# Kernel optimization log

Measured on AMD Instinct MI355X. Metric: run time of the kernel, lower is better.

## Reference

```python
import jax, jax.numpy as jnp
import numpy as np

EPS = 1e-3  # keras LayerNormalization default epsilon


def setup_inputs() -> dict:
    key = jax.random.key(0)
    ks = jax.random.split(key, 6)
    B, T, D, U = 128, 512, 512, 512
    scale = 1.0 / np.sqrt(U + D)
    return {
        "x": jax.random.normal(ks[0], (B, T, D), jnp.float32),
        "h0": jnp.zeros((B, U), jnp.float32),
        "c0": jnp.zeros((B, U), jnp.float32),
        "Wf": jax.random.normal(ks[1], (U, U + D), jnp.float32) * scale,
        "bf": jnp.zeros((U,), jnp.float32),
        "Wg": jax.random.normal(ks[2], (U, U + D), jnp.float32) * scale,
        "bg": jnp.zeros((U,), jnp.float32),
        "Wi": jax.random.normal(ks[3], (U, U + D), jnp.float32) * scale,
        "bi": jnp.zeros((U,), jnp.float32),
        "Wo": jax.random.normal(ks[4], (U, U + D), jnp.float32) * scale,
        "bo": jnp.zeros((U,), jnp.float32),
        "gamma": jnp.ones((U,), jnp.float32),
        "beta": jnp.zeros((U,), jnp.float32),
    }


def reference(x, h0, c0, Wf, bf, Wg, bg, Wi, bi, Wo, bo, gamma, beta):
    # Stack the 4 gate weights/biases: one GEMM per step instead of four.
    W = jnp.stack([Wf, Wg, Wi, Wo])          # [4, U, U+D]
    b = jnp.stack([bf, bg, bi, bo])          # [4, U]

    def ln(z):
        # shared LayerNormalization over the last (units) axis
        m = jnp.mean(z, axis=-1, keepdims=True)
        v = jnp.var(z, axis=-1, keepdims=True)
        return (z - m) * jax.lax.rsqrt(v + EPS) * gamma + beta

    def step(carry, xt):
        h, c = carry                          # [B, U] each
        cat = jnp.concatenate([h, xt], axis=-1)   # [B, U+D]
        z = jnp.einsum('bd,gud->bgu', cat, W) + b  # [B, 4, U]
        z = ln(z)                             # LN per gate over units
        f = jax.nn.sigmoid(z[:, 0])
        g = jnp.tanh(z[:, 1])
        i = jax.nn.sigmoid(z[:, 2])
        o = jax.nn.sigmoid(z[:, 3])
        c_new = c * f + g * i
        c_ln = ln(c_new)                      # layer_norm_c_state: carried c is normalized
        h_new = o * jnp.tanh(c_ln)
        return (h_new, c_ln), h_new

    xs = jnp.swapaxes(x, 0, 1)                # [T, B, D]
    (_, _), hs = jax.lax.scan(step, (h0, c0), xs)
    return jnp.swapaxes(hs, 0, 1)             # [B, T, U]
```

## Files before the change

kernel.cpp:

```cpp
#include <hip/hip_runtime.h>
#include <hip/hip_fp16.h>


typedef unsigned short ushort_t;
typedef unsigned long long u64;
typedef __attribute__((ext_vector_type(8))) short short8;
typedef __attribute__((ext_vector_type(4))) float f32x4;

#define Bsz 128
#define Tn  512
#define Un  512
#define NU  2048
#define NC  16
#define WPC 16
#define BPC 8

#define GIDX(u) ((u) + ((u) >> 5))

__device__ __forceinline__ ushort_t f2bf(float f){
  unsigned u = __float_as_uint(f);
  u = u + 0x7fffu + ((u >> 16) & 1u);
  return (ushort_t)(u >> 16);
}
__device__ __forceinline__ float bf2f(ushort_t h){
  return __uint_as_float(((unsigned)h) << 16);
}
__device__ __forceinline__ float sigf(float x){ return 1.0f/(1.0f + __expf(-x)); }
__device__ __forceinline__ float tanh_fast(float x){
  float ax = fabsf(x);
  float e  = __expf(-2.0f*ax);
  float r  = (1.0f - e)/(1.0f + e);
  return x >= 0.0f ? r : -r;
}

__device__ __forceinline__ void st_tag(u64* p, float v, unsigned tag){
  u64 w = ((u64)tag << 32) | (u64)__float_as_uint(v);
  __hip_atomic_store(p, w, __ATOMIC_RELAXED, __HIP_MEMORY_SCOPE_AGENT);
}
__device__ __forceinline__ void st_u64(u64* p, u64 w){
  __hip_atomic_store(p, w, __ATOMIC_RELAXED, __HIP_MEMORY_SCOPE_AGENT);
}
__device__ __forceinline__ void st_f32(float* p, float v){
  __hip_atomic_store(p, v, __ATOMIC_RELAXED, __HIP_MEMORY_SCOPE_AGENT);
}
__device__ __forceinline__ u64 ld_u64(const u64* p){
  return __hip_atomic_load(p, __ATOMIC_RELAXED, __HIP_MEMORY_SCOPE_AGENT);
}
__device__ __forceinline__ float lo_f(u64 w){ return __uint_as_float((unsigned)w); }
__device__ __forceinline__ float hi_f(u64 w){ return __uint_as_float((unsigned)(w >> 32)); }

__global__ void k_prep_w(const float* __restrict__ Wf, const float* __restrict__ Wg,
                         const float* __restrict__ Wi, const float* __restrict__ Wo,
                         ushort_t* __restrict__ wh_hi, ushort_t* __restrict__ wh_lo){
  int idx = blockIdx.x*blockDim.x + threadIdx.x;
  if (idx >= 1048576) return;
  const float* Wp[4] = {Wf, Wg, Wi, Wo};
  int j = idx & 7;
  int lane = (idx >> 3) & 63;
  int i = (idx >> 9) & 31;
  int wslot = idx >> 14;
  int kiter = i >> 1, nt = i & 1;
  int wid = wslot >> 2, wave = wslot & 3;
  int n = wid*128 + wave*32 + nt*16 + (lane & 15);
  int k = kiter*32 + (lane >> 4)*8 + j;
  int gate = n >> 9, u = n & 511;
  float w = Wp[gate][u*1024 + k];
  ushort_t hi = f2bf(w);
  wh_hi[idx] = hi;
  wh_lo[idx] = f2bf(w - bf2f(hi));
}

__global__ __launch_bounds__(256,2) void k_gemm_xz(const float* __restrict__ A,
    const float* __restrict__ Wf, const float* __restrict__ Wg,
    const float* __restrict__ Wi, const float* __restrict__ Wo,
    __half* __restrict__ C){
  __shared__ __align__(16) ushort_t Ah[128*32];
  __shared__ __align__(16) ushort_t Al[128*32];
  __shared__ __align__(16) ushort_t Bh[128*32];
  __shared__ __align__(16) ushort_t Bl[128*32];
  const int tid  = threadIdx.x;
  const int lane = tid & 63, wave = tid >> 6;
  const int quad = lane >> 4, l15 = lane & 15;
  const int wm = wave >> 1, wn = wave & 1;
  const int m0 = blockIdx.x * 128, n0 = blockIdx.y * 128;
  const float* Wp = (n0 < 512) ? Wf : (n0 < 1024) ? Wg : (n0 < 1536) ? Wi : Wo;
  const int u0 = n0 & 511;
  f32x4 acc[4][4];
  #pragma unroll
  for (int a=0;a<4;a++)
    #pragma unroll
    for (int b=0;b<4;b++) acc[a][b] = (f32x4){0.f,0.f,0.f,0.f};

  for (int kc = 0; kc < 512; kc += 32){
    __syncthreads();
    #pragma unroll
    for (int p=0; p<4; p++){
      int slot = p*256 + tid;
      int row = slot >> 3, seg = slot & 7;
      float4 va = *(const float4*)(A  + (size_t)(m0+row)*512  + kc + seg*4);
      float4 vb = *(const float4*)(Wp + (size_t)(u0+row)*1024 + 512 + kc + seg*4);
      ushort4 ah, al, bh, bl;
      ah.x=f2bf(va.x); al.x=f2bf(va.x-bf2f(ah.x));
      ah.y=f2bf(va.y); al.y=f2bf(va.y-bf2f(ah.y));
      ah.z=f2bf(va.z); al.z=f2bf(va.z-bf2f(ah.z));
      ah.w=f2bf(va.w); al.w=f2bf(va.w-bf2f(ah.w));
      bh.x=f2bf(vb.x); bl.x=f2bf(vb.x-bf2f(bh.x));
      bh.y=f2bf(vb.y); bl.y=f2bf(vb.y-bf2f(bh.y));
      bh.z=f2bf(vb.z); bl.z=f2bf(vb.z-bf2f(bh.z));
      bh.w=f2bf(vb.w); bl.w=f2bf(vb.w-bf2f(bh.w));
      *(ushort4*)(Ah + slot*4) = ah;
      *(ushort4*)(Al + slot*4) = al;
      *(ushort4*)(Bh + slot*4) = bh;
      *(ushort4*)(Bl + slot*4) = bl;
    }
    __syncthreads();
    short8 afh[4], afl[4], bfh[4], bfl[4];
    #pragma unroll
    for (int ti=0; ti<4; ti++){
      afh[ti] = *(const short8*)(Ah + (wm*64 + ti*16 + l15)*32 + quad*8);
      afl[ti] = *(const short8*)(Al + (wm*64 + ti*16 + l15)*32 + quad*8);
    }
    #pragma unroll
    for (int tj=0; tj<4; tj++){
      bfh[tj] = *(const short8*)(Bh + (wn*64 + tj*16 + l15)*32 + quad*8);
      bfl[tj] = *(const short8*)(Bl + (wn*64 + tj*16 + l15)*32 + quad*8);
    }
    #pragma unroll
    for (int ti=0; ti<4; ti++)
      #pragma unroll
      for (int tj=0; tj<4; tj++){
        acc[ti][tj] = __builtin_amdgcn_mfma_f32_16x16x32_bf16(afh[ti], bfh[tj], acc[ti][tj], 0,0,0);
        acc[ti][tj] = __builtin_amdgcn_mfma_f32_16x16x32_bf16(afl[ti], bfh[tj], acc[ti][tj], 0,0,0);
        acc[ti][tj] = __builtin_amdgcn_mfma_f32_16x16x32_bf16(afh[ti], bfl[tj], acc[ti][tj], 0,0,0);
      }
  }
  #pragma unroll
  for (int ti=0; ti<4; ti++)
    #pragma unroll
    for (int tj=0; tj<4; tj++)
      #pragma unroll
      for (int r=0; r<4; r++){
        int m = m0 + wm*64 + ti*16 + quad*4 + r;
        int n = n0 + wn*64 + tj*16 + l15;
        C[(size_t)m*NU + n] = __float2half(acc[ti][tj][r]);
      }
}

__global__ __launch_bounds__(256,1) void k_lstm(
    const ushort_t* __restrict__ wh_hi_g, const ushort_t* __restrict__ wh_lo_g,
    const __half* __restrict__ xz,
    const float* __restrict__ bfp, const float* __restrict__ bgp,
    const float* __restrict__ bip, const float* __restrict__ bop,
    const float* __restrict__ gamma, const float* __restrict__ beta,
    const float* __restrict__ h0, const float* __restrict__ c0,
    float* __restrict__ actf, u64* __restrict__ zbuf,
    u64* __restrict__ zflag, u64* __restrict__ aflag,
    float* __restrict__ out)
{
  const int bid = blockIdx.x;
  const int cid = bid & 15;
  const int wid = bid >> 4;
  const int tid = threadIdx.x;
  const int wave = tid >> 6, lane = tid & 63;
  const int quad = lane >> 4, l15 = lane & 15;
  const int gate = wid >> 2;

  __shared__ __align__(16) ushort_t h_hi[16][520];
  __shared__ __align__(16) ushort_t h_lo[16][520];
  __shared__ float gamma_lds[528], beta_lds[528];
  __shared__ float wavepart[4][8][2];

  for (int i = tid; i < 16*520; i += 256){
    int r = i / 520, u = i - r*520;
    float v = (r < BPC && u < 512) ? h0[(cid*BPC + r)*512 + u] : 0.0f;
    ushort_t hh = f2bf(v);
    h_hi[r][u] = hh;
    h_lo[r][u] = f2bf(v - bf2f(hh));
  }
  for (int i = tid; i < 512; i += 256){ gamma_lds[GIDX(i)] = gamma[i]; beta_lds[GIDX(i)] = beta[i]; }

  const int b_loc = tid >> 5;
  const int l2 = (tid & 31) << 1;
  float c[16];
  #pragma unroll
  for (int i=0;i<16;i++) c[i] = c0[(cid*BPC + b_loc)*512 + (i>>1)*64 + l2 + (i&1)];

  short8 wrh[32], wrl[32];
  {
    const ushort_t* wph = wh_hi_g + (size_t)(wid*4 + wave)*16384 + lane*8;
    const ushort_t* wpl = wh_lo_g + (size_t)(wid*4 + wave)*16384 + lane*8;
    #pragma unroll
    for (int i=0;i<32;i++){
      wrh[i] = *(const short8*)(wph + (size_t)i*512);
      wrl[i] = *(const short8*)(wpl + (size_t)i*512);
    }
  }

  float bias_r[2], gam_r[2], bet_r[2];
  int ng_[2];
  #pragma unroll
  for (int nt=0; nt<2; nt++){
    int ng = wid*128 + wave*32 + nt*16 + l15;
    ng_[nt] = ng;
    int u = ng & 511;
    const float* bp = (gate==0)? bfp : (gate==1)? bgp : (gate==2)? bip : bop;
    bias_r[nt] = bp[u];
    gam_r[nt] = gamma[u]; bet_r[nt] = beta[u];
  }
  const bool bvalid = (quad < 2);
  const int b_base = quad*4;

  const size_t fbase0 = (size_t)(0*NC + cid)*WPC;
  const size_t fbase1 = (size_t)(1*NC + cid)*WPC;

  __syncthreads();

  for (int t = 0; t < Tn; ++t){
    const unsigned tag = (unsigned)(t + 1);
    const int par = t & 1;
    const size_t fb = par ? fbase1 : fbase0;
    float xzv[2][4];
    #pragma unroll
    for (int nt=0; nt<2; nt++)
      #pragma unroll
      for (int r=0; r<4; r++){
        if (bvalid){
          int b = cid*BPC + b_base + r;
          xzv[nt][r] = __half2float(xz[((size_t)b*Tn + t)*NU + ng_[nt]]);
        } else xzv[nt][r] = 0.0f;
      }
    f32x4 acc0 = (f32x4){0.f,0.f,0.f,0.f}, acc1 = (f32x4){0.f,0.f,0.f,0.f};
    #pragma unroll
    for (int ki=0; ki<16; ki++){
      short8 afh = *(const short8*)(&h_hi[l15][ki*32 + quad*8]);
      short8 afl = *(const short8*)(&h_lo[l15][ki*32 + quad*8]);
      acc0 = __builtin_amdgcn_mfma_f32_16x16x32_bf16(afh, wrh[2*ki+0], acc0, 0,0,0);
      acc0 = __builtin_amdgcn_mfma_f32_16x16x32_bf16(afl, wrh[2*ki+0], acc0, 0,0,0);
      acc0 = __builtin_amdgcn_mfma_f32_16x16x32_bf16(afh, wrl[2*ki+0], acc0, 0,0,0);
      acc1 = __builtin_amdgcn_mfma_f32_16x16x32_bf16(afh, wrh[2*ki+1], acc1, 0,0,0);
      acc1 = __builtin_amdgcn_mfma_f32_16x16x32_bf16(afl, wrh[2*ki+1], acc1, 0,0,0);
      acc1 = __builtin_amdgcn_mfma_f32_16x16x32_bf16(afh, wrl[2*ki+1], acc1, 0,0,0);
    }
    float z[2][4];
    #pragma unroll
    for (int r=0;r<4;r++){
      z[0][r] = bvalid ? (acc0[r] + xzv[0][r] + bias_r[0]) : 0.0f;
      z[1][r] = bvalid ? (acc1[r] + xzv[1][r] + bias_r[1]) : 0.0f;
    }
    float sum[4], ssq[4];
    #pragma unroll
    for (int r=0;r<4;r++){
      float s = z[0][r] + z[1][r];
      float q = z[0][r]*z[0][r] + z[1][r]*z[1][r];
      #pragma unroll
      for (int off=1; off<16; off<<=1){ s += __shfl_xor(s, off); q += __shfl_xor(q, off); }
      sum[r]=s; ssq[r]=q;
    }
    if (l15 == 0 && bvalid){
      #pragma unroll
      for (int r=0;r<4;r++){
        wavepart[wave][b_base + r][0] = sum[r];
        wavepart[wave][b_base + r][1] = ssq[r];
      }
    }
    __syncthreads();
    if (tid < 8){
      float S = wavepart[0][tid][0] + wavepart[1][tid][0] + wavepart[2][tid][0] + wavepart[3][tid][0];
      float Q = wavepart[0][tid][1] + wavepart[1][tid][1] + wavepart[2][tid][1] + wavepart[3][tid][1];
      u64 w = ((u64)__float_as_uint(Q) << 32) | (u64)__float_as_uint(S);
      st_u64(zbuf + fb*BPC + (size_t)wid*BPC + tid, w);
    }
    asm volatile("s_waitcnt vmcnt(0)" ::: "memory");
    __syncthreads();
    if (tid == 0) st_tag(zflag + fb + wid, 0.0f, tag);
    if (tid < 4 && (gate*4 + tid) != wid){
      const u64* fp = zflag + fb + gate*4 + tid;
      while ((unsigned)(ld_u64(fp) >> 32) != tag) { }
    }
    __syncthreads();

    if (bvalid){
      float Ssum[4], Qsum[4];
      #pragma unroll
      for (int r=0;r<4;r++){ Ssum[r]=0.f; Qsum[r]=0.f; }
      u64 zw[4][4];
      #pragma unroll
      for (int j=0;j<4;j++)
        #pragma unroll
        for (int r=0;r<4;r++)
          zw[j][r] = ld_u64(zbuf + fb*BPC + (size_t)(gate*4+j)*BPC + b_base + r);
      #pragma unroll
      for (int j=0;j<4;j++)
        #pragma unroll
        for (int r=0;r<4;r++){ Ssum[r] += lo_f(zw[j][r]); Qsum[r] += hi_f(zw[j][r]); }
      #pragma unroll
      for (int r=0;r<4;r++){
        float m_ = Ssum[r] * (1.0f/512.0f);
        float var = Qsum[r] * (1.0f/512.0f) - m_*m_;
        float rstd = rsqrtf(var + 1e-3f);
        #pragma unroll
        for (int nt=0;nt<2;nt++){
          float zn = (z[nt][r] - m_) * rstd * gam_r[nt] + bet_r[nt];
          float a = (gate==1) ? tanh_fast(zn) : sigf(zn);
          st_f32(actf + (size_t)((par*NC + cid)*BPC + b_base + r)*NU + ng_[nt], a);
        }
      }
    }
    asm volatile("s_waitcnt vmcnt(0)" ::: "memory");
    __syncthreads();
    if (tid == 0) st_tag(aflag + fb + wid, 0.0f, tag);
    if (tid < 16 && tid != wid){
      const u64* fp = aflag + fb + tid;
      while ((unsigned)(ld_u64(fp) >> 32) != tag) { }
    }
    __syncthreads();

    {
      const float* abf = actf + (size_t)((par*NC + cid)*BPC + b_loc)*NU;
      float cn[16], og[16];
      float ls = 0.f, lq = 0.f;
      #pragma unroll
      for (int ch=0; ch<2; ch++){
        u64 w[4][4];
        #pragma unroll
        for (int g=0; g<4; g++)
          #pragma unroll
          for (int jj=0; jj<4; jj++)
            w[g][jj] = ld_u64((const u64*)(abf + (size_t)g*512 + (ch*4+jj)*64 + l2));
        #pragma unroll
        for (int jj=0; jj<4; jj++)
          #pragma unroll
          for (int e=0; e<2; e++){
            int k = ch*8 + jj*2 + e;
            float fv = e ? hi_f(w[0][jj]) : lo_f(w[0][jj]);
            float gv = e ? hi_f(w[1][jj]) : lo_f(w[1][jj]);
            float iv = e ? hi_f(w[2][jj]) : lo_f(w[2][jj]);
            float ov = e ? hi_f(w[3][jj]) : lo_f(w[3][jj]);
            float cv = c[k]*fv + gv*iv;
            cn[k] = cv;
            og[k] = ov;
            ls += cv; lq += cv*cv;
          }
      }
      #pragma unroll
      for (int off=1; off<32; off<<=1){ ls += __shfl_xor(ls, off); lq += __shfl_xor(lq, off); }
      float m_ = ls*(1.0f/512.0f);
      float var = lq*(1.0f/512.0f) - m_*m_;
      float rs = rsqrtf(var + 1e-3f);
      #pragma unroll
      for (int j=0; j<8; j++){
        int u0 = j*64 + l2;
        float cl0 = (cn[2*j+0]-m_)*rs*gamma_lds[GIDX(u0)]   + beta_lds[GIDX(u0)];
        float cl1 = (cn[2*j+1]-m_)*rs*gamma_lds[GIDX(u0+1)] + beta_lds[GIDX(u0+1)];
        c[2*j+0] = cl0; c[2*j+1] = cl1;
        float hv0 = og[2*j+0]*tanh_fast(cl0);
        float hv1 = og[2*j+1]*tanh_fast(cl1);
        ushort2 hh; hh.x = f2bf(hv0); hh.y = f2bf(hv1);
        ushort2 hl; hl.x = f2bf(hv0 - bf2f(hh.x)); hl.y = f2bf(hv1 - bf2f(hh.y));
        *(ushort2*)&h_hi[b_loc][u0] = hh;
        *(ushort2*)&h_lo[b_loc][u0] = hl;
        if (wid == 0){
          float2 hv; hv.x = hv0; hv.y = hv1;
          *(float2*)&out[((size_t)(cid*BPC + b_loc)*Tn + t)*Un + u0] = hv;
        }
      }
    }
    __syncthreads();
  }
}

extern "C" void kernel_launch(void* const* d_in, const int* in_sizes, int n_in,
                              void* d_out, int out_size, void* d_ws, size_t ws_size,
                              hipStream_t stream){
  const float* x     = (const float*)d_in[0];
  const float* h0    = (const float*)d_in[1];
  const float* c0    = (const float*)d_in[2];
  const float* Wf    = (const float*)d_in[3];
  const float* bf_   = (const float*)d_in[4];
  const float* Wg    = (const float*)d_in[5];
  const float* bg_   = (const float*)d_in[6];
  const float* Wi    = (const float*)d_in[7];
  const float* bi_   = (const float*)d_in[8];
  const float* Wo    = (const float*)d_in[9];
  const float* bo_   = (const float*)d_in[10];
  const float* gamma = (const float*)d_in[11];
  const float* beta  = (const float*)d_in[12];

  char* ws = (char*)d_ws;
  __half*   xz    = (__half*)(ws);
  ushort_t* wh_hi = (ushort_t*)(ws + (256ull<<20));
  ushort_t* wh_lo = (ushort_t*)(ws + (258ull<<20));
  float*    actf  = (float*)(ws + (260ull<<20));
  u64*      zbuf  = (u64*)(ws + (262ull<<20));
  u64*      zflag = (u64*)(ws + (262ull<<20) + (32ull<<10));
  u64*      aflag = (u64*)(ws + (262ull<<20) + (36ull<<10));
  float* out = (float*)d_out;

  hipMemsetAsync(zflag, 0, 8ull<<10, stream);
  k_prep_w<<<4096, 256, 0, stream>>>(Wf, Wg, Wi, Wo, wh_hi, wh_lo);
  dim3 g(Bsz*Tn/128, NU/128);
  k_gemm_xz<<<g, 256, 0, stream>>>(x, Wf, Wg, Wi, Wo, xz);
  k_lstm<<<256, 256, 0, stream>>>(wh_hi, wh_lo, xz, bf_, bg_, bi_, bo_, gamma, beta, h0, c0,
                                  actf, zbuf, zflag, aflag, out);
}
```

Baseline: 6.212 ms.

## Split recurrent LSTM work across 512 blocks with 32 workgroups per batch chunk

Doubles the number of persistent workgroups per batch cluster from 16 to 32, so each block handles 64 gate columns instead of 128. Per-step MFMA work and register-resident weights per wave are halved, and launch bounds allow two blocks per CU. The cost is more cross-block flag polling per step (8 z-flags and 32 activation flags) and more global synchronisation traffic, and all 512 blocks must be co-resident for the spin barriers not to deadlock.

```diff
diff --git a/kernel.cpp b/kernel.cpp
--- a/kernel.cpp
+++ b/kernel.cpp
@@ -12,7 +12,7 @@
 #define Un  512
 #define NU  2048
 #define NC  16
-#define WPC 16
+#define WPC 32
 #define BPC 8
 
 #define GIDX(u) ((u) + ((u) >> 5))
@@ -55,15 +55,14 @@
   int idx = blockIdx.x*blockDim.x + threadIdx.x;
   if (idx >= 1048576) return;
   const float* Wp[4] = {Wf, Wg, Wi, Wo};
-  int j = idx & 7;
+  int j    = idx & 7;
   int lane = (idx >> 3) & 63;
-  int i = (idx >> 9) & 31;
-  int wslot = idx >> 14;
-  int kiter = i >> 1, nt = i & 1;
-  int wid = wslot >> 2, wave = wslot & 3;
-  int n = wid*128 + wave*32 + nt*16 + (lane & 15);
-  int k = kiter*32 + (lane >> 4)*8 + j;
-  int gate = n >> 9, u = n & 511;
+  int ki   = (idx >> 9) & 15;
+  int wave = (idx >> 13) & 3;
+  int wid  = idx >> 15;
+  int gate = wid >> 3;
+  int u = (wid & 7)*64 + wave*16 + (lane & 15);
+  int k = ki*32 + (lane >> 4)*8 + j;
   float w = Wp[gate][u*1024 + k];
   ushort_t hi = f2bf(w);
   wh_hi[idx] = hi;
@@ -146,7 +145,7 @@
       }
 }
 
-__global__ __launch_bounds__(256,1) void k_lstm(
+__global__ __launch_bounds__(256,2) void k_lstm(
     const ushort_t* __restrict__ wh_hi_g, const ushort_t* __restrict__ wh_lo_g,
     const __half* __restrict__ xz,
     const float* __restrict__ bfp, const float* __restrict__ bgp,
@@ -158,12 +157,12 @@
     float* __restrict__ out)
 {
   const int bid = blockIdx.x;
-  const int cid = bid & 15;
-  const int wid = bid >> 4;
+  const int cid = bid >> 5;
+  const int wid = bid & 31;
   const int tid = threadIdx.x;
   const int wave = tid >> 6, lane = tid & 63;
   const int quad = lane >> 4, l15 = lane & 15;
-  const int gate = wid >> 2;
+  const int gate = wid >> 3;
 
   __shared__ __align__(16) ushort_t h_hi[16][520];
   __shared__ __align__(16) ushort_t h_lo[16][520];
@@ -185,73 +184,61 @@
   #pragma unroll
   for (int i=0;i<16;i++) c[i] = c0[(cid*BPC + b_loc)*512 + (i>>1)*64 + l2 + (i&1)];
 
-  short8 wrh[32], wrl[32];
+  short8 wrh[16], wrl[16];
   {
-    const ushort_t* wph = wh_hi_g + (size_t)(wid*4 + wave)*16384 + lane*8;
-    const ushort_t* wpl = wh_lo_g + (size_t)(wid*4 + wave)*16384 + lane*8;
-    #pragma unroll
-    for (int i=0;i<32;i++){
+    const ushort_t* wph = wh_hi_g + (size_t)(wid*4 + wave)*8192 + lane*8;
+    const ushort_t* wpl = wh_lo_g + (size_t)(wid*4 + wave)*8192 + lane*8;
+    #pragma unroll
+    for (int i=0;i<16;i++){
       wrh[i] = *(const short8*)(wph + (size_t)i*512);
       wrl[i] = *(const short8*)(wpl + (size_t)i*512);
     }
   }
 
-  float bias_r[2], gam_r[2], bet_r[2];
-  int ng_[2];
-  #pragma unroll
-  for (int nt=0; nt<2; nt++){
-    int ng = wid*128 + wave*32 + nt*16 + l15;
-    ng_[nt] = ng;
-    int u = ng & 511;
+  const int ng = wid*64 + wave*16 + l15;
+  const int uu = ng & 511;
+  float bias_r, gam_r, bet_r;
+  {
     const float* bp = (gate==0)? bfp : (gate==1)? bgp : (gate==2)? bip : bop;
-    bias_r[nt] = bp[u];
-    gam_r[nt] = gamma[u]; bet_r[nt] = beta[u];
+    bias_r = bp[uu];
+    gam_r = gamma[uu]; bet_r = beta[uu];
   }
   const bool bvalid = (quad < 2);
   const int b_base = quad*4;
-
-  const size_t fbase0 = (size_t)(0*NC + cid)*WPC;
-  const size_t fbase1 = (size_t)(1*NC + cid)*WPC;
 
   __syncthreads();
 
   for (int t = 0; t < Tn; ++t){
     const unsigned tag = (unsigned)(t + 1);
     const int par = t & 1;
-    const size_t fb = par ? fbase1 : fbase0;
-    float xzv[2][4];
-    #pragma unroll
-    for (int nt=0; nt<2; nt++)
-      #pragma unroll
-      for (int r=0; r<4; r++){
-        if (bvalid){
-          int b = cid*BPC + b_base + r;
-          xzv[nt][r] = __half2float(xz[((size_t)b*Tn + t)*NU + ng_[nt]]);
-        } else xzv[nt][r] = 0.0f;
-      }
-    f32x4 acc0 = (f32x4){0.f,0.f,0.f,0.f}, acc1 = (f32x4){0.f,0.f,0.f,0.f};
+    const size_t fb = (size_t)(par*NC + cid)*WPC;
+    float xzv[4];
+    #pragma unroll
+    for (int r=0; r<4; r++){
+      if (bvalid){
+        int b = cid*BPC + b_base + r;
+        xzv[r] = __half2float(xz[((size_t)b*Tn + t)*NU + ng]);
+      } else xzv[r] = 0.0f;
+    }
+    f32x4 acc = (f32x4){0.f,0.f,0.f,0.f};
     #pragma unroll
     for (int ki=0; ki<16; ki++){
       short8 afh = *(const short8*)(&h_hi[l15][ki*32 + quad*8]);
       short8 afl = *(const short8*)(&h_lo[l15][ki*32 + quad*8]);
-      acc0 = __builtin_amdgcn_mfma_f32_16x16x32_bf16(afh, wrh[2*ki+0], acc0, 0,0,0);
-      acc0 = __builtin_amdgcn_mfma_f32_16x16x32_bf16(afl, wrh[2*ki+0], acc0, 0,0,0);
-      acc0 = __builtin_amdgcn_mfma_f32_16x16x32_bf16(afh, wrl[2*ki+0], acc0, 0,0,0);
-      acc1 = __builtin_amdgcn_mfma_f32_16x16x32_bf16(afh, wrh[2*ki+1], acc1, 0,0,0);
-      acc1 = __builtin_amdgcn_mfma_f32_16x16x32_bf16(afl, wrh[2*ki+1], acc1, 0,0,0);
-      acc1 = __builtin_amdgcn_mfma_f32_16x16x32_bf16(afh, wrl[2*ki+1], acc1, 0,0,0);
-    }
-    float z[2][4];
+      acc = __builtin_amdgcn_mfma_f32_16x16x32_bf16(afh, wrh[ki], acc, 0,0,0);
+      acc = __builtin_amdgcn_mfma_f32_16x16x32_bf16(afl, wrh[ki], acc, 0,0,0);
+      acc = __builtin_amdgcn_mfma_f32_16x16x32_bf16(afh, wrl[ki], acc, 0,0,0);
+    }
+    float z[4];
+    #pragma unroll
+    for (int r=0;r<4;r++)
+      z[r] = bvalid ? (acc[r] + xzv[r] + bias_r) : 0.0f;
+
+    float sum[4], ssq[4];
     #pragma unroll
     for (int r=0;r<4;r++){
-      z[0][r] = bvalid ? (acc0[r] + xzv[0][r] + bias_r[0]) : 0.0f;
-      z[1][r] = bvalid ? (acc1[r] + xzv[1][r] + bias_r[1]) : 0.0f;
-    }
-    float sum[4], ssq[4];
-    #pragma unroll
-    for (int r=0;r<4;r++){
-      float s = z[0][r] + z[1][r];
-      float q = z[0][r]*z[0][r] + z[1][r]*z[1][r];
+      float s = z[r];
+      float q = z[r]*z[r];
       #pragma unroll
       for (int off=1; off<16; off<<=1){ s += __shfl_xor(s, off); q += __shfl_xor(q, off); }
       sum[r]=s; ssq[r]=q;
@@ -268,13 +255,13 @@
       float S = wavepart[0][tid][0] + wavepart[1][tid][0] + wavepart[2][tid][0] + wavepart[3][tid][0];
       float Q = wavepart[0][tid][1] + wavepart[1][tid][1] + wavepart[2][tid][1] + wavepart[3][tid][1];
       u64 w = ((u64)__float_as_uint(Q) << 32) | (u64)__float_as_uint(S);
-      st_u64(zbuf + fb*BPC + (size_t)wid*BPC + tid, w);
+      st_u64(zbuf + (fb + wid)*BPC + tid, w);
     }
     asm volatile("s_waitcnt vmcnt(0)" ::: "memory");
     __syncthreads();
     if (tid == 0) st_tag(zflag + fb + wid, 0.0f, tag);
-    if (tid < 4 && (gate*4 + tid) != wid){
-      const u64* fp = zflag + fb + gate*4 + tid;
+    if (tid < 8 && (gate*8 + tid) != wid){
+      const u64* fp = zflag + fb + gate*8 + tid;
       while ((unsigned)(ld_u64(fp) >> 32) != tag) { }
     }
     __syncthreads();
@@ -283,33 +270,33 @@
       float Ssum[4], Qsum[4];
       #pragma unroll
       for (int r=0;r<4;r++){ Ssum[r]=0.f; Qsum[r]=0.f; }
-      u64 zw[4][4];
-      #pragma unroll
-      for (int j=0;j<4;j++)
+      #pragma unroll
+      for (int jh=0; jh<2; jh++){
+        u64 zw[4][4];
         #pragma unroll
-        for (int r=0;r<4;r++)
-          zw[j][r] = ld_u64(zbuf + fb*BPC + (size_t)(gate*4+j)*BPC + b_base + r);
-      #pragma unroll
-      for (int j=0;j<4;j++)
+        for (int jj=0;jj<4;jj++)
+          #pragma unroll
+          for (int r=0;r<4;r++)
+            zw[jj][r] = ld_u64(zbuf + (fb + gate*8 + jh*4 + jj)*BPC + b_base + r);
         #pragma unroll
-        for (int r=0;r<4;r++){ Ssum[r] += lo_f(zw[j][r]); Qsum[r] += hi_f(zw[j][r]); }
+        for (int jj=0;jj<4;jj++)
+          #pragma unroll
+          for (int r=0;r<4;r++){ Ssum[r] += lo_f(zw[jj][r]); Qsum[r] += hi_f(zw[jj][r]); }
+      }
       #pragma unroll
       for (int r=0;r<4;r++){
         float m_ = Ssum[r] * (1.0f/512.0f);
         float var = Qsum[r] * (1.0f/512.0f) - m_*m_;
         float rstd = rsqrtf(var + 1e-3f);
-        #pragma unroll
-        for (int nt=0;nt<2;nt++){
-          float zn = (z[nt][r] - m_) * rstd * gam_r[nt] + bet_r[nt];
-          float a = (gate==1) ? tanh_fast(zn) : sigf(zn);
-          st_f32(actf + (size_t)((par*NC + cid)*BPC + b_base + r)*NU + ng_[nt], a);
-        }
+        float zn = (z[r] - m_) * rstd * gam_r + bet_r;
+        float a = (gate==1) ? tanh_fast(zn) : sigf(zn);
+        st_f32(actf + (size_t)((par*NC + cid)*BPC + b_base + r)*NU + ng, a);
       }
     }
     asm volatile("s_waitcnt vmcnt(0)" ::: "memory");
     __syncthreads();
     if (tid == 0) st_tag(aflag + fb + wid, 0.0f, tag);
-    if (tid < 16 && tid != wid){
+    if (tid < 32 && tid != wid){
       const u64* fp = aflag + fb + tid;
       while ((unsigned)(ld_u64(fp) >> 32) != tag) { }
     }
@@ -392,14 +379,14 @@
   ushort_t* wh_lo = (ushort_t*)(ws + (258ull<<20));
   float*    actf  = (float*)(ws + (260ull<<20));
   u64*      zbuf  = (u64*)(ws + (262ull<<20));
-  u64*      zflag = (u64*)(ws + (262ull<<20) + (32ull<<10));
-  u64*      aflag = (u64*)(ws + (262ull<<20) + (36ull<<10));
+  u64*      zflag = (u64*)(ws + (262ull<<20) + (64ull<<10));
+  u64*      aflag = (u64*)(ws + (262ull<<20) + (72ull<<10));
   float* out = (float*)d_out;
 
-  hipMemsetAsync(zflag, 0, 8ull<<10, stream);
+  hipMemsetAsync(zflag, 0, 16ull<<10, stream);
   k_prep_w<<<4096, 256, 0, stream>>>(Wf, Wg, Wi, Wo, wh_hi, wh_lo);
   dim3 g(Bsz*Tn/128, NU/128);
   k_gemm_xz<<<g, 256, 0, stream>>>(x, Wf, Wg, Wi, Wo, xz);
-  k_lstm<<<256, 256, 0, stream>>>(wh_hi, wh_lo, xz, bf_, bg_, bi_, bo_, gamma, beta, h0, c0,
+  k_lstm<<<512, 256, 0, stream>>>(wh_hi, wh_lo, xz, bf_, bg_, bi_, bo_, gamma, beta, h0, c0,
                                   actf, zbuf, zflag, aflag, out);
 }
```

Result: slower. 7.648 ms (+23.1%).

## Exchange raw gate pre-activations to drop one cross-block barrier per step

Applied to the files above, without the earlier changes.

Each of the 16 workgroups in a batch cluster now writes its raw gate pre-activations to global memory and waits on a single flag barrier across all 16 workgroups. Every workgroup then recomputes the per-gate layer-norm statistics and activations itself for its batch rows. Before, there were two grid barriers per timestep: one for the partial LN sums and one for the activations. This removes one inter-workgroup spin-wait round per step, at the cost of redundant LN and transcendental work and wider waits on all 16 flags.

```diff
diff --git a/kernel.cpp b/kernel.cpp
--- a/kernel.cpp
+++ b/kernel.cpp
@@ -35,9 +35,6 @@
 
 __device__ __forceinline__ void st_tag(u64* p, float v, unsigned tag){
   u64 w = ((u64)tag << 32) | (u64)__float_as_uint(v);
-  __hip_atomic_store(p, w, __ATOMIC_RELAXED, __HIP_MEMORY_SCOPE_AGENT);
-}
-__device__ __forceinline__ void st_u64(u64* p, u64 w){
   __hip_atomic_store(p, w, __ATOMIC_RELAXED, __HIP_MEMORY_SCOPE_AGENT);
 }
 __device__ __forceinline__ void st_f32(float* p, float v){
@@ -153,8 +150,7 @@
     const float* __restrict__ bip, const float* __restrict__ bop,
     const float* __restrict__ gamma, const float* __restrict__ beta,
     const float* __restrict__ h0, const float* __restrict__ c0,
-    float* __restrict__ actf, u64* __restrict__ zbuf,
-    u64* __restrict__ zflag, u64* __restrict__ aflag,
+    float* __restrict__ zex, u64* __restrict__ zflag,
     float* __restrict__ out)
 {
   const int bid = blockIdx.x;
@@ -168,7 +164,6 @@
   __shared__ __align__(16) ushort_t h_hi[16][520];
   __shared__ __align__(16) ushort_t h_lo[16][520];
   __shared__ float gamma_lds[528], beta_lds[528];
-  __shared__ float wavepart[4][8][2];
 
   for (int i = tid; i < 16*520; i += 256){
     int r = i / 520, u = i - r*520;
@@ -196,7 +191,7 @@
     }
   }
 
-  float bias_r[2], gam_r[2], bet_r[2];
+  float bias_r[2];
   int ng_[2];
   #pragma unroll
   for (int nt=0; nt<2; nt++){
@@ -205,20 +200,16 @@
     int u = ng & 511;
     const float* bp = (gate==0)? bfp : (gate==1)? bgp : (gate==2)? bip : bop;
     bias_r[nt] = bp[u];
-    gam_r[nt] = gamma[u]; bet_r[nt] = beta[u];
   }
   const bool bvalid = (quad < 2);
   const int b_base = quad*4;
-
-  const size_t fbase0 = (size_t)(0*NC + cid)*WPC;
-  const size_t fbase1 = (size_t)(1*NC + cid)*WPC;
 
   __syncthreads();
 
   for (int t = 0; t < Tn; ++t){
     const unsigned tag = (unsigned)(t + 1);
     const int par = t & 1;
-    const size_t fb = par ? fbase1 : fbase0;
+    const size_t fb = (size_t)(par*NC + cid)*WPC;
     float xzv[2][4];
     #pragma unroll
     for (int nt=0; nt<2; nt++)
@@ -241,107 +232,75 @@
       acc1 = __builtin_amdgcn_mfma_f32_16x16x32_bf16(afl, wrh[2*ki+1], acc1, 0,0,0);
       acc1 = __builtin_amdgcn_mfma_f32_16x16x32_bf16(afh, wrl[2*ki+1], acc1, 0,0,0);
     }
-    float z[2][4];
-    #pragma unroll
-    for (int r=0;r<4;r++){
-      z[0][r] = bvalid ? (acc0[r] + xzv[0][r] + bias_r[0]) : 0.0f;
-      z[1][r] = bvalid ? (acc1[r] + xzv[1][r] + bias_r[1]) : 0.0f;
-    }
-    float sum[4], ssq[4];
-    #pragma unroll
-    for (int r=0;r<4;r++){
-      float s = z[0][r] + z[1][r];
-      float q = z[0][r]*z[0][r] + z[1][r]*z[1][r];
-      #pragma unroll
-      for (int off=1; off<16; off<<=1){ s += __shfl_xor(s, off); q += __shfl_xor(q, off); }
-      sum[r]=s; ssq[r]=q;
-    }
-    if (l15 == 0 && bvalid){
+    if (bvalid){
       #pragma unroll
       for (int r=0;r<4;r++){
-        wavepart[wave][b_base + r][0] = sum[r];
-        wavepart[wave][b_base + r][1] = ssq[r];
-      }
-    }
-    __syncthreads();
-    if (tid < 8){
-      float S = wavepart[0][tid][0] + wavepart[1][tid][0] + wavepart[2][tid][0] + wavepart[3][tid][0];
-      float Q = wavepart[0][tid][1] + wavepart[1][tid][1] + wavepart[2][tid][1] + wavepart[3][tid][1];
-      u64 w = ((u64)__float_as_uint(Q) << 32) | (u64)__float_as_uint(S);
-      st_u64(zbuf + fb*BPC + (size_t)wid*BPC + tid, w);
+        float z0 = acc0[r] + xzv[0][r] + bias_r[0];
+        float z1 = acc1[r] + xzv[1][r] + bias_r[1];
+        float* zp = zex + (size_t)((par*NC + cid)*BPC + b_base + r)*NU;
+        st_f32(zp + ng_[0], z0);
+        st_f32(zp + ng_[1], z1);
+      }
     }
     asm volatile("s_waitcnt vmcnt(0)" ::: "memory");
     __syncthreads();
     if (tid == 0) st_tag(zflag + fb + wid, 0.0f, tag);
-    if (tid < 4 && (gate*4 + tid) != wid){
-      const u64* fp = zflag + fb + gate*4 + tid;
+    if (tid < WPC && tid != wid){
+      const u64* fp = zflag + fb + tid;
       while ((unsigned)(ld_u64(fp) >> 32) != tag) { }
     }
     __syncthreads();
 
-    if (bvalid){
-      float Ssum[4], Qsum[4];
-      #pragma unroll
-      for (int r=0;r<4;r++){ Ssum[r]=0.f; Qsum[r]=0.f; }
-      u64 zw[4][4];
-      #pragma unroll
-      for (int j=0;j<4;j++)
-        #pragma unroll
-        for (int r=0;r<4;r++)
-          zw[j][r] = ld_u64(zbuf + fb*BPC + (size_t)(gate*4+j)*BPC + b_base + r);
-      #pragma unroll
-      for (int j=0;j<4;j++)
-        #pragma unroll
-        for (int r=0;r<4;r++){ Ssum[r] += lo_f(zw[j][r]); Qsum[r] += hi_f(zw[j][r]); }
-      #pragma unroll
-      for (int r=0;r<4;r++){
-        float m_ = Ssum[r] * (1.0f/512.0f);
-        float var = Qsum[r] * (1.0f/512.0f) - m_*m_;
-        float rstd = rsqrtf(var + 1e-3f);
-        #pragma unroll
-        for (int nt=0;nt<2;nt++){
-          float zn = (z[nt][r] - m_) * rstd * gam_r[nt] + bet_r[nt];
-          float a = (gate==1) ? tanh_fast(zn) : sigf(zn);
-          st_f32(actf + (size_t)((par*NC + cid)*BPC + b_base + r)*NU + ng_[nt], a);
-        }
-      }
-    }
-    asm volatile("s_waitcnt vmcnt(0)" ::: "memory");
-    __syncthreads();
-    if (tid == 0) st_tag(aflag + fb + wid, 0.0f, tag);
-    if (tid < 16 && tid != wid){
-      const u64* fp = aflag + fb + tid;
-      while ((unsigned)(ld_u64(fp) >> 32) != tag) { }
-    }
-    __syncthreads();
-
     {
-      const float* abf = actf + (size_t)((par*NC + cid)*BPC + b_loc)*NU;
-      float cn[16], og[16];
-      float ls = 0.f, lq = 0.f;
-      #pragma unroll
-      for (int ch=0; ch<2; ch++){
-        u64 w[4][4];
+      const float* zbf = zex + (size_t)((par*NC + cid)*BPC + b_loc)*NU;
+      u64 zv[2][4][4];
+      #pragma unroll
+      for (int ch=0; ch<2; ch++)
         #pragma unroll
         for (int g=0; g<4; g++)
           #pragma unroll
           for (int jj=0; jj<4; jj++)
-            w[g][jj] = ld_u64((const u64*)(abf + (size_t)g*512 + (ch*4+jj)*64 + l2));
+            zv[ch][g][jj] = ld_u64((const u64*)(zbf + (size_t)g*512 + (ch*4+jj)*64 + l2));
+      float mg[4], rg[4];
+      #pragma unroll
+      for (int g=0; g<4; g++){
+        float s=0.f, q=0.f;
+        #pragma unroll
+        for (int ch=0; ch<2; ch++)
+          #pragma unroll
+          for (int jj=0; jj<4; jj++){
+            float a = lo_f(zv[ch][g][jj]), b = hi_f(zv[ch][g][jj]);
+            s += a + b; q += a*a + b*b;
+          }
+        #pragma unroll
+        for (int off=1; off<32; off<<=1){ s += __shfl_xor(s, off); q += __shfl_xor(q, off); }
+        float m_ = s*(1.0f/512.0f);
+        float v_ = q*(1.0f/512.0f) - m_*m_;
+        mg[g] = m_; rg[g] = rsqrtf(v_ + 1e-3f);
+      }
+      float cn[16], og[16];
+      float ls = 0.f, lq = 0.f;
+      #pragma unroll
+      for (int ch=0; ch<2; ch++)
         #pragma unroll
         for (int jj=0; jj<4; jj++)
           #pragma unroll
           for (int e=0; e<2; e++){
             int k = ch*8 + jj*2 + e;
-            float fv = e ? hi_f(w[0][jj]) : lo_f(w[0][jj]);
-            float gv = e ? hi_f(w[1][jj]) : lo_f(w[1][jj]);
-            float iv = e ? hi_f(w[2][jj]) : lo_f(w[2][jj]);
-            float ov = e ? hi_f(w[3][jj]) : lo_f(w[3][jj]);
+            int u0 = (ch*4+jj)*64 + l2 + e;
+            float gam = gamma_lds[GIDX(u0)], bet = beta_lds[GIDX(u0)];
+            float zf = e ? hi_f(zv[ch][0][jj]) : lo_f(zv[ch][0][jj]);
+            float zg = e ? hi_f(zv[ch][1][jj]) : lo_f(zv[ch][1][jj]);
+            float zi = e ? hi_f(zv[ch][2][jj]) : lo_f(zv[ch][2][jj]);
+            float zo = e ? hi_f(zv[ch][3][jj]) : lo_f(zv[ch][3][jj]);
+            float fv = sigf     ((zf - mg[0])*rg[0]*gam + bet);
+            float gv = tanh_fast((zg - mg[1])*rg[1]*gam + bet);
+            float iv = sigf     ((zi - mg[2])*rg[2]*gam + bet);
+            float ov = sigf     ((zo - mg[3])*rg[3]*gam + bet);
             float cv = c[k]*fv + gv*iv;
-            cn[k] = cv;
-            og[k] = ov;
+            cn[k] = cv; og[k] = ov;
             ls += cv; lq += cv*cv;
           }
-      }
       #pragma unroll
       for (int off=1; off<32; off<<=1){ ls += __shfl_xor(ls, off); lq += __shfl_xor(lq, off); }
       float m_ = ls*(1.0f/512.0f);
@@ -390,16 +349,14 @@
   __half*   xz    = (__half*)(ws);
   ushort_t* wh_hi = (ushort_t*)(ws + (256ull<<20));
   ushort_t* wh_lo = (ushort_t*)(ws + (258ull<<20));
-  float*    actf  = (float*)(ws + (260ull<<20));
-  u64*      zbuf  = (u64*)(ws + (262ull<<20));
-  u64*      zflag = (u64*)(ws + (262ull<<20) + (32ull<<10));
-  u64*      aflag = (u64*)(ws + (262ull<<20) + (36ull<<10));
+  float*    zex   = (float*)(ws + (260ull<<20));
+  u64*      zflag = (u64*)(ws + (262ull<<20));
   float* out = (float*)d_out;
 
-  hipMemsetAsync(zflag, 0, 8ull<<10, stream);
+  hipMemsetAsync(zflag, 0, 4ull<<10, stream);
   k_prep_w<<<4096, 256, 0, stream>>>(Wf, Wg, Wi, Wo, wh_hi, wh_lo);
   dim3 g(Bsz*Tn/128, NU/128);
   k_gemm_xz<<<g, 256, 0, stream>>>(x, Wf, Wg, Wi, Wo, xz);
   k_lstm<<<256, 256, 0, stream>>>(wh_hi, wh_lo, xz, bf_, bg_, bi_, bo_, gamma, beta, h0, c0,
-                                  actf, zbuf, zflag, aflag, out);
-}
+                                  zex, zflag, out);
+}
```

After: 6.356 ms. 1.02x slower.

## Replace LN-stat flag barrier with tag-embedded partial sums polled directly

Applied to the files above, without the earlier changes.

The per-step exchange of layer-norm partial sums between the four blocks of a gate previously used a data store, a vmcnt drain, a barrier, a separate flag store and a spin on flags. Now each sum and sum-of-squares is stored with the step tag in its upper 32 bits, and readers poll the data words until all tags match, which removes one barrier and one global round trip per step. It also moves gamma/beta for the c-state LayerNorm from LDS into registers and swaps the divisions in sigmoid/tanh for hardware reciprocal. The risks are more polling traffic on the data words, extra register pressure in a kernel that already keeps its weights in registers, and slightly lower precision from rcp.

```diff
diff --git a/kernel.cpp b/kernel.cpp
--- a/kernel.cpp
+++ b/kernel.cpp
@@ -15,8 +15,6 @@
 #define WPC 16
 #define BPC 8
 
-#define GIDX(u) ((u) + ((u) >> 5))
-
 __device__ __forceinline__ ushort_t f2bf(float f){
   unsigned u = __float_as_uint(f);
   u = u + 0x7fffu + ((u >> 16) & 1u);
@@ -25,19 +23,19 @@
 __device__ __forceinline__ float bf2f(ushort_t h){
   return __uint_as_float(((unsigned)h) << 16);
 }
-__device__ __forceinline__ float sigf(float x){ return 1.0f/(1.0f + __expf(-x)); }
+__device__ __forceinline__ float sigf(float x){
+  float e = __expf(-x);
+  return __builtin_amdgcn_rcpf(1.0f + e);
+}
 __device__ __forceinline__ float tanh_fast(float x){
   float ax = fabsf(x);
   float e  = __expf(-2.0f*ax);
-  float r  = (1.0f - e)/(1.0f + e);
+  float r  = (1.0f - e) * __builtin_amdgcn_rcpf(1.0f + e);
   return x >= 0.0f ? r : -r;
 }
 
 __device__ __forceinline__ void st_tag(u64* p, float v, unsigned tag){
   u64 w = ((u64)tag << 32) | (u64)__float_as_uint(v);
-  __hip_atomic_store(p, w, __ATOMIC_RELAXED, __HIP_MEMORY_SCOPE_AGENT);
-}
-__device__ __forceinline__ void st_u64(u64* p, u64 w){
   __hip_atomic_store(p, w, __ATOMIC_RELAXED, __HIP_MEMORY_SCOPE_AGENT);
 }
 __device__ __forceinline__ void st_f32(float* p, float v){
@@ -153,8 +151,8 @@
     const float* __restrict__ bip, const float* __restrict__ bop,
     const float* __restrict__ gamma, const float* __restrict__ beta,
     const float* __restrict__ h0, const float* __restrict__ c0,
-    float* __restrict__ actf, u64* __restrict__ zbuf,
-    u64* __restrict__ zflag, u64* __restrict__ aflag,
+    float* __restrict__ actf, u64* __restrict__ zpart,
+    u64* __restrict__ aflag,
     float* __restrict__ out)
 {
   const int bid = blockIdx.x;
@@ -167,7 +165,6 @@
 
   __shared__ __align__(16) ushort_t h_hi[16][520];
   __shared__ __align__(16) ushort_t h_lo[16][520];
-  __shared__ float gamma_lds[528], beta_lds[528];
   __shared__ float wavepart[4][8][2];
 
   for (int i = tid; i < 16*520; i += 256){
@@ -177,13 +174,17 @@
     h_hi[r][u] = hh;
     h_lo[r][u] = f2bf(v - bf2f(hh));
   }
-  for (int i = tid; i < 512; i += 256){ gamma_lds[GIDX(i)] = gamma[i]; beta_lds[GIDX(i)] = beta[i]; }
 
   const int b_loc = tid >> 5;
   const int l2 = (tid & 31) << 1;
   float c[16];
+  float gam16[16], bet16[16];
   #pragma unroll
-  for (int i=0;i<16;i++) c[i] = c0[(cid*BPC + b_loc)*512 + (i>>1)*64 + l2 + (i&1)];
+  for (int i=0;i<16;i++){
+    int u = (i>>1)*64 + l2 + (i&1);
+    c[i] = c0[(cid*BPC + b_loc)*512 + u];
+    gam16[i] = gamma[u]; bet16[i] = beta[u];
+  }
 
   short8 wrh[32], wrl[32];
   {
@@ -210,15 +211,12 @@
   const bool bvalid = (quad < 2);
   const int b_base = quad*4;
 
-  const size_t fbase0 = (size_t)(0*NC + cid)*WPC;
-  const size_t fbase1 = (size_t)(1*NC + cid)*WPC;
-
   __syncthreads();
 
   for (int t = 0; t < Tn; ++t){
     const unsigned tag = (unsigned)(t + 1);
     const int par = t & 1;
-    const size_t fb = par ? fbase1 : fbase0;
+    const size_t fb = (size_t)(par*NC + cid)*WPC;
     float xzv[2][4];
     #pragma unroll
     for (int nt=0; nt<2; nt++)
@@ -267,36 +265,41 @@
     if (tid < 8){
       float S = wavepart[0][tid][0] + wavepart[1][tid][0] + wavepart[2][tid][0] + wavepart[3][tid][0];
       float Q = wavepart[0][tid][1] + wavepart[1][tid][1] + wavepart[2][tid][1] + wavepart[3][tid][1];
-      u64 w = ((u64)__float_as_uint(Q) << 32) | (u64)__float_as_uint(S);
-      st_u64(zbuf + fb*BPC + (size_t)wid*BPC + tid, w);
-    }
-    asm volatile("s_waitcnt vmcnt(0)" ::: "memory");
-    __syncthreads();
-    if (tid == 0) st_tag(zflag + fb + wid, 0.0f, tag);
-    if (tid < 4 && (gate*4 + tid) != wid){
-      const u64* fp = zflag + fb + gate*4 + tid;
-      while ((unsigned)(ld_u64(fp) >> 32) != tag) { }
+      u64* zp = zpart + ((fb + wid)*BPC + tid)*2;
+      st_tag(zp+0, S, tag);
+      st_tag(zp+1, Q, tag);
     }
     __syncthreads();
 
     if (bvalid){
-      float Ssum[4], Qsum[4];
-      #pragma unroll
-      for (int r=0;r<4;r++){ Ssum[r]=0.f; Qsum[r]=0.f; }
-      u64 zw[4][4];
+      u64 zv[16][2];
       #pragma unroll
       for (int j=0;j<4;j++)
         #pragma unroll
-        for (int r=0;r<4;r++)
-          zw[j][r] = ld_u64(zbuf + fb*BPC + (size_t)(gate*4+j)*BPC + b_base + r);
-      #pragma unroll
-      for (int j=0;j<4;j++)
+        for (int r=0;r<4;r++){
+          const u64* zp = zpart + ((fb + gate*4 + j)*BPC + b_base + r)*2;
+          zv[j*4+r][0] = ld_u64(zp+0);
+          zv[j*4+r][1] = ld_u64(zp+1);
+        }
+      unsigned miss;
+      do {
+        miss = 0u;
         #pragma unroll
-        for (int r=0;r<4;r++){ Ssum[r] += lo_f(zw[j][r]); Qsum[r] += hi_f(zw[j][r]); }
+        for (int j=0;j<4;j++)
+          #pragma unroll
+          for (int r=0;r<4;r++){
+            const u64* zp = zpart + ((fb + gate*4 + j)*BPC + b_base + r)*2;
+            if ((unsigned)(zv[j*4+r][0] >> 32) != tag){ zv[j*4+r][0] = ld_u64(zp+0); miss = 1u; }
+            if ((unsigned)(zv[j*4+r][1] >> 32) != tag){ zv[j*4+r][1] = ld_u64(zp+1); miss = 1u; }
+          }
+        if (miss) __builtin_amdgcn_s_sleep(1);
+      } while (miss);
       #pragma unroll
       for (int r=0;r<4;r++){
-        float m_ = Ssum[r] * (1.0f/512.0f);
-        float var = Qsum[r] * (1.0f/512.0f) - m_*m_;
+        float S = lo_f(zv[0*4+r][0]) + lo_f(zv[1*4+r][0]) + lo_f(zv[2*4+r][0]) + lo_f(zv[3*4+r][0]);
+        float Q = lo_f(zv[0*4+r][1]) + lo_f(zv[1*4+r][1]) + lo_f(zv[2*4+r][1]) + lo_f(zv[3*4+r][1]);
+        float m_ = S * (1.0f/512.0f);
+        float var = Q * (1.0f/512.0f) - m_*m_;
         float rstd = rsqrtf(var + 1e-3f);
         #pragma unroll
         for (int nt=0;nt<2;nt++){
@@ -350,8 +353,8 @@
       #pragma unroll
       for (int j=0; j<8; j++){
         int u0 = j*64 + l2;
-        float cl0 = (cn[2*j+0]-m_)*rs*gamma_lds[GIDX(u0)]   + beta_lds[GIDX(u0)];
-        float cl1 = (cn[2*j+1]-m_)*rs*gamma_lds[GIDX(u0+1)] + beta_lds[GIDX(u0+1)];
+        float cl0 = (cn[2*j+0]-m_)*rs*gam16[2*j+0] + bet16[2*j+0];
+        float cl1 = (cn[2*j+1]-m_)*rs*gam16[2*j+1] + bet16[2*j+1];
         c[2*j+0] = cl0; c[2*j+1] = cl1;
         float hv0 = og[2*j+0]*tanh_fast(cl0);
         float hv1 = og[2*j+1]*tanh_fast(cl1);
@@ -391,15 +394,14 @@
   ushort_t* wh_hi = (ushort_t*)(ws + (256ull<<20));
   ushort_t* wh_lo = (ushort_t*)(ws + (258ull<<20));
   float*    actf  = (float*)(ws + (260ull<<20));
-  u64*      zbuf  = (u64*)(ws + (262ull<<20));
-  u64*      zflag = (u64*)(ws + (262ull<<20) + (32ull<<10));
-  u64*      aflag = (u64*)(ws + (262ull<<20) + (36ull<<10));
+  u64*      zpart = (u64*)(ws + (262ull<<20));
+  u64*      aflag = (u64*)(ws + (262ull<<20) + (64ull<<10));
   float* out = (float*)d_out;
 
-  hipMemsetAsync(zflag, 0, 8ull<<10, stream);
+  hipMemsetAsync(zpart, 0, (64ull<<10) + (4ull<<10), stream);
   k_prep_w<<<4096, 256, 0, stream>>>(Wf, Wg, Wi, Wo, wh_hi, wh_lo);
   dim3 g(Bsz*Tn/128, NU/128);
   k_gemm_xz<<<g, 256, 0, stream>>>(x, Wf, Wg, Wi, Wo, xz);
   k_lstm<<<256, 256, 0, stream>>>(wh_hi, wh_lo, xz, bf_, bg_, bi_, bo_, gamma, beta, h0, c0,
-                                  actf, zbuf, zflag, aflag, out);
-}
+                                  actf, zpart, aflag, out);
+}
```

New measurement: 6.435 ms. 1.04x slower.
